# Kernel tuning notes

Hardware: AMD Instinct MI355X
Metric: run time of the kernel (lower is better)

The kernel has to match this reference:

```python
import jax, jax.numpy as jnp
import numpy as np

N = 20000   # nodes per graph
E = 320000  # edges per graph
D_IN, D_H = 128, 304


def _param(key, shape, fan_in):
    return jax.random.normal(key, shape, dtype=jnp.float32) / np.sqrt(fan_in)


def setup_inputs() -> dict:
    key = jax.random.key(0)
    ks = jax.random.split(key, 20)
    inp = {}
    for i, name in enumerate(['x1', 'x2', 'x3']):
        inp[name] = jax.random.normal(ks[i], (N, D_IN), dtype=jnp.float32)
    for i, name in enumerate(['src1', 'dst1', 'src2', 'dst2', 'src3', 'dst3']):
        inp[name] = jax.random.randint(ks[3 + i], (E,), 0, N, dtype=jnp.int32)
    # shared GraphConv weights (DGL GraphConv: h = norm_agg(x) @ W + b)
    inp['W1'] = _param(ks[9], (D_IN, D_H), D_IN)
    inp['b1'] = jnp.zeros((D_H,), jnp.float32)
    inp['W2'] = _param(ks[10], (D_H, D_H), D_H)
    inp['b2'] = jnp.zeros((D_H,), jnp.float32)
    inp['W3'] = _param(ks[11], (D_H, D_H), D_H)
    inp['b3'] = jnp.zeros((D_H,), jnp.float32)
    # MLP head: 304 -> 128 -> 64 -> 1
    inp['fW1'] = _param(ks[12], (D_H, 128), D_H)
    inp['fb1'] = jnp.zeros((128,), jnp.float32)
    inp['fW2'] = _param(ks[13], (128, 64), 128)
    inp['fb2'] = jnp.zeros((64,), jnp.float32)
    inp['fW3'] = _param(ks[14], (64, 1), 64)
    inp['fb3'] = jnp.zeros((1,), jnp.float32)
    return inp


def gcn_conv(x, src, dst, W, b):
    # DGL GraphConv, norm='both': h = D_in^{-1/2} A D_out^{-1/2} x W + b
    ones = jnp.ones((src.shape[0],), x.dtype)
    out_deg = jnp.clip(jax.ops.segment_sum(ones, src, num_segments=N), 1.0)
    in_deg = jnp.clip(jax.ops.segment_sum(ones, dst, num_segments=N), 1.0)
    h = x * jax.lax.rsqrt(out_deg)[:, None]
    agg = jax.ops.segment_sum(h[src], dst, num_segments=N)  # [N, d] SpMM
    agg = agg * jax.lax.rsqrt(in_deg)[:, None]
    return agg @ W + b


def reference(x1, x2, x3, src1, dst1, src2, dst2, src3, dst3,
              W1, b1, W2, b2, W3, b3, fW1, fb1, fW2, fb2, fW3, fb3):
    def branch(x, src, dst):
        x = jax.nn.relu(gcn_conv(x, src, dst, W1, b1))
        x = jax.nn.relu(gcn_conv(x, src, dst, W2, b2))
        x = jax.nn.relu(gcn_conv(x, src, dst, W3, b3))
        return x

    h1 = branch(x1, src1, dst1)
    h2 = branch(x2, src2, dst2)
    h3 = branch(x3, src3, dst3)
    # multi_graph_opt='max': max over all nodes of all three graphs -> [304]
    pooled = jnp.max(jnp.concatenate([h1, h2, h3], axis=0), axis=0)
    # output_opt='fc': MLP head with sigmoid
    z = jax.nn.relu(pooled @ fW1 + fb1)
    z = jax.nn.relu(z @ fW2 + fb2)
    return jax.nn.sigmoid(z @ fW3 + fb3)  # shape [1]
```

## Files before the change

### kernel.cpp

```cpp
#include <hip/hip_runtime.h>
#include <hip/hip_bf16.h>
#include <math.h>

#define NODES 20000
#define EDGES 320000
#define NB 3
#define TOTN (NODES * NB)
#define TOTE (EDGES * NB)
#define D_IN 128
#define D_H 304
#define SCAN_B 59
#define SLICES 40
#define SLICE_E (EDGES / SLICES)
#define ZX TOTN
#define ZQ (TOTN + 96)
#define OFFB 237
#define PACKB 7500
#define PREPWB 912

typedef __attribute__((ext_vector_type(4))) float f32x4;
typedef __attribute__((ext_vector_type(2))) float f32x2;

__device__ __forceinline__ void gload16(const void* g, void* l) {
    __builtin_amdgcn_global_load_lds(
        (const __attribute__((address_space(1))) unsigned*)g,
        (__attribute__((address_space(3))) unsigned*)l, 16, 0, 0);
}

__global__ __launch_bounds__(256, 1) void k_hist(
    const int* __restrict__ s1, const int* __restrict__ d1,
    const int* __restrict__ s2, const int* __restrict__ d2,
    const int* __restrict__ s3, const int* __restrict__ d3,
    unsigned short* __restrict__ partial_in, unsigned short* __restrict__ partial_out,
    int* __restrict__ gctr) {
    __shared__ unsigned hist[NODES / 2];
    if (blockIdx.x == 0 && blockIdx.y == 0 && threadIdx.x == 0) *gctr = 0;
    int g = blockIdx.x / SLICES, s = blockIdx.x % SLICES;
    bool isOut = (blockIdx.y == 1);
    const int* ep;
    if (isOut) ep = (g == 0) ? s1 : ((g == 1) ? s2 : s3);
    else       ep = (g == 0) ? d1 : ((g == 1) ? d2 : d3);
    ep += s * SLICE_E;
    for (int i = threadIdx.x; i < NODES / 2; i += 256) hist[i] = 0;
    __syncthreads();
    const int4* ep4 = (const int4*)ep;
    for (int i = threadIdx.x; i < SLICE_E / 4; i += 256) {
        int4 v = ep4[i];
        atomicAdd(&hist[v.x >> 1], 1u << ((v.x & 1) << 4));
        atomicAdd(&hist[v.y >> 1], 1u << ((v.y & 1) << 4));
        atomicAdd(&hist[v.z >> 1], 1u << ((v.z & 1) << 4));
        atomicAdd(&hist[v.w >> 1], 1u << ((v.w & 1) << 4));
    }
    __syncthreads();
    unsigned* po = (unsigned*)((isOut ? partial_out : partial_in) + (size_t)blockIdx.x * NODES);
    for (int i = threadIdx.x; i < NODES / 2; i += 256) po[i] = hist[i];
}

__global__ void k_degscan(const unsigned short* __restrict__ partial_in,
                          const unsigned short* __restrict__ partial_out,
                          float* __restrict__ inv_in, float* __restrict__ inv_out,
                          int* __restrict__ row_ptr, int* __restrict__ rend,
                          int* __restrict__ gctr) {
    __shared__ int wsum[16];
    __shared__ int sbase;
    int b = blockIdx.x, t = threadIdx.x;
    int i = b * 1024 + t;
    int lane = t & 63, wid = t >> 6;
    int v = 0;
    if (i < TOTN) {
        int g = i / NODES, ln = i - g * NODES;
        const unsigned short* pi = partial_in + (size_t)g * SLICES * NODES + ln;
        const unsigned short* po = partial_out + (size_t)g * SLICES * NODES + ln;
        int ci = 0, co = 0;
        #pragma unroll
        for (int s = 0; s < SLICES; s++) { ci += pi[s * NODES]; co += po[s * NODES]; }
        v = ci;
        inv_in[i]  = 1.0f / sqrtf((float)max(ci, 1));
        inv_out[i] = 1.0f / sqrtf((float)max(co, 1));
    }
    int sv = v;
    #pragma unroll
    for (int o = 1; o < 64; o <<= 1) {
        int u = __shfl_up(sv, o, 64);
        if (lane >= o) sv += u;
    }
    if (lane == 63) wsum[wid] = sv;
    __syncthreads();
    if (t < 16) {
        int w = wsum[t];
        #pragma unroll
        for (int o = 1; o < 16; o <<= 1) {
            int u = __shfl_up(w, o, 16);
            if (t >= o) w += u;
        }
        wsum[t] = w;
    }
    __syncthreads();
    if (t == 0) sbase = atomicAdd(gctr, wsum[15]);
    __syncthreads();
    int wbase = (wid > 0) ? wsum[wid - 1] : 0;
    if (i < TOTN) {
        int rp = sbase + wbase + sv - v;
        row_ptr[i] = rp;
        rend[i] = rp + v;
    }
}

__global__ void k_prep(const int* __restrict__ row_ptr,
                       const unsigned short* __restrict__ partial_in,
                       int* __restrict__ O,
                       int* __restrict__ csr_slack, unsigned* __restrict__ x8z,
                       unsigned* __restrict__ q8z, int* __restrict__ pooled,
                       const float4* __restrict__ x1, const float4* __restrict__ x2,
                       const float4* __restrict__ x3, const float* __restrict__ inv_out,
                       unsigned* __restrict__ q,
                       const float* __restrict__ W1, const float* __restrict__ W2,
                       const float* __restrict__ W3,
                       unsigned char* __restrict__ Wt1, unsigned char* __restrict__ Wt2,
                       unsigned char* __restrict__ Wt3) {
    if (blockIdx.x < OFFB) {
        int n = blockIdx.x * 256 + threadIdx.x;
        if (n >= TOTN) {
            int ex = n - TOTN;
            if (ex < 32) csr_slack[ex] = 0;
            else if (ex < 64) x8z[ex - 32] = 0;
            else if (ex < 144) q8z[ex - 64] = 0;
            else if (ex < 464) pooled[ex - 144] = 0;
            return;
        }
        int rp = row_ptr[n];
        int g = n / NODES, ln = n - g * NODES;
        const unsigned short* pi = partial_in + (size_t)g * SLICES * NODES + ln;
        int* on = O + (size_t)g * SLICES * NODES + ln;
        int run = rp;
        #pragma unroll
        for (int s = 0; s < SLICES; s++) {
            on[s * NODES] = run;
            run += pi[s * NODES];
        }
    } else if (blockIdx.x < OFFB + PACKB) {
        const int per = NODES * D_IN / 4;
        int i = (blockIdx.x - OFFB) * 256 + threadIdx.x;
        const float4* s; int j;
        if (i < per)          { s = x1; j = i; }
        else if (i < 2 * per) { s = x2; j = i - per; }
        else                  { s = x3; j = i - 2 * per; }
        float4 v = s[j];
        float sc = inv_out[i >> 5];
        int p = __builtin_amdgcn_cvt_pk_fp8_f32(v.x * sc, v.y * sc, 0, false);
        p = __builtin_amdgcn_cvt_pk_fp8_f32(v.z * sc, v.w * sc, p, true);
        q[i] = (unsigned)p;
    } else {
        const int N1 = D_H * 128, N2 = D_H * 320;
        int id = (blockIdx.x - OFFB - PACKB) * 256 + threadIdx.x;
        const float* W; unsigned char* Wt; int K, Kpad, lid;
        if (id < N1)                { W = W1; Wt = Wt1; K = 128; Kpad = 128; lid = id; }
        else if (id < N1 + N2)      { W = W2; Wt = Wt2; K = 304; Kpad = 320; lid = id - N1; }
        else                        { W = W3; Wt = Wt3; K = 304; Kpad = 320; lid = id - N1 - N2; }
        int n = lid / Kpad, k = lid - n * Kpad;
        unsigned char v = 0;
        if (k < K) {
            float w = W[k * D_H + n];
            v = (unsigned char)(__builtin_amdgcn_cvt_pk_fp8_f32(w, w, 0, false) & 0xff);
        }
        Wt[lid] = v;
    }
}

__global__ __launch_bounds__(256, 1) void k_fill2(
    const int* __restrict__ s1, const int* __restrict__ d1,
    const int* __restrict__ s2, const int* __restrict__ d2,
    const int* __restrict__ s3, const int* __restrict__ d3,
    const int* __restrict__ O, int* __restrict__ csr) {
    __shared__ int cur[NODES];
    int g = blockIdx.x / SLICES, s = blockIdx.x % SLICES;
    const int* sp = (g == 0) ? s1 : ((g == 1) ? s2 : s3);
    const int* dp = (g == 0) ? d1 : ((g == 1) ? d2 : d3);
    sp += s * SLICE_E; dp += s * SLICE_E;
    const int* on = O + (size_t)blockIdx.x * NODES;
    for (int i = threadIdx.x; i < NODES; i += 256) cur[i] = on[i];
    __syncthreads();
    int base = g * NODES;
    const int4* sp4 = (const int4*)sp;
    const int4* dp4 = (const int4*)dp;
    for (int i = threadIdx.x; i < SLICE_E / 4; i += 256) {
        int4 dv = dp4[i];
        int4 sv = sp4[i];
        int p0 = atomicAdd(&cur[dv.x], 1); csr[p0] = sv.x + base;
        int p1 = atomicAdd(&cur[dv.y], 1); csr[p1] = sv.y + base;
        int p2 = atomicAdd(&cur[dv.z], 1); csr[p2] = sv.z + base;
        int p3 = atomicAdd(&cur[dv.w], 1); csr[p3] = sv.w + base;
    }
}

__global__ void k_spmm_l1(const uint2* __restrict__ h, unsigned char* __restrict__ agg,
                          const int* __restrict__ row_ptr, const int* __restrict__ rend,
                          const int* __restrict__ csr,
                          const float* __restrict__ inv_in) {
    int n = blockIdx.x * 4 + (threadIdx.x >> 6);
    int lane = threadIdx.x & 63;
    int s = lane >> 4;
    int off = lane & 15;
    f32x2 a[4];
    #pragma unroll
    for (int j = 0; j < 4; j++) a[j] = (f32x2){0.f, 0.f};
    int k0 = row_ptr[n], k1 = rend[n];
    int deg = k1 - k0;
    const int* cp = csr + k0 + s;
    int e[8];
    #pragma unroll
    for (int j = 0; j < 8; j++) {
        int ev = cp[4 * j];
        e[j] = (s + 4 * j < deg) ? ev : ZX;
    }
    uint2 u[8];
    #pragma unroll
    for (int j = 0; j < 8; j++)
        if (4 * j < deg) u[j] = h[(size_t)e[j] * 16 + off];
    #pragma unroll
    for (int j = 0; j < 8; j++) {
        if (4 * j < deg) {
            a[0] += __builtin_amdgcn_cvt_pk_f32_fp8(u[j].x, false);
            a[1] += __builtin_amdgcn_cvt_pk_f32_fp8(u[j].x, true);
            a[2] += __builtin_amdgcn_cvt_pk_f32_fp8(u[j].y, false);
            a[3] += __builtin_amdgcn_cvt_pk_f32_fp8(u[j].y, true);
        }
    }
    for (int k = k0 + 32 + s; k < k1; k += 4) {
        int e0 = csr[k];
        uint2 u0 = h[(size_t)e0 * 16 + off];
        a[0] += __builtin_amdgcn_cvt_pk_f32_fp8(u0.x, false);
        a[1] += __builtin_amdgcn_cvt_pk_f32_fp8(u0.x, true);
        a[2] += __builtin_amdgcn_cvt_pk_f32_fp8(u0.y, false);
        a[3] += __builtin_amdgcn_cvt_pk_f32_fp8(u0.y, true);
    }
    float r[8];
    #pragma unroll
    for (int j = 0; j < 4; j++) {
        #pragma unroll
        for (int c = 0; c < 2; c++) {
            float v = a[j][c];
            r[2 * j + c] = v + __shfl(v, lane + 16, 64)
                             + __shfl(v, lane + 32, 64)
                             + __shfl(v, lane + 48, 64);
        }
    }
    if (lane < 16) {
        float wi = inv_in[n];
        int d0 = __builtin_amdgcn_cvt_pk_fp8_f32(r[0] * wi, r[1] * wi, 0, false);
        d0 = __builtin_amdgcn_cvt_pk_fp8_f32(r[2] * wi, r[3] * wi, d0, true);
        int d1 = __builtin_amdgcn_cvt_pk_fp8_f32(r[4] * wi, r[5] * wi, 0, false);
        d1 = __builtin_amdgcn_cvt_pk_fp8_f32(r[6] * wi, r[7] * wi, d1, true);
        uint2 st; st.x = (unsigned)d0; st.y = (unsigned)d1;
        *(uint2*)(agg + (size_t)n * 128 + lane * 8) = st;
    }
}

__global__ void k_spmm_big(const uint4* __restrict__ h, unsigned char* __restrict__ agg,
                           const int* __restrict__ row_ptr, const int* __restrict__ rend,
                           const int* __restrict__ csr,
                           const float* __restrict__ inv_in) {
    int n = blockIdx.x * 4 + (threadIdx.x >> 6);
    int lane = threadIdx.x & 63;
    int s = lane / 20;
    int off = lane % 20;
    f32x2 a[8];
    #pragma unroll
    for (int j = 0; j < 8; j++) a[j] = (f32x2){0.f, 0.f};
    int k0 = row_ptr[n], k1 = rend[n];
    int deg = k1 - k0;
    int degg = (s < 3) ? deg : 0;
    const int* cp = csr + k0 + s;
    int e[8];
    #pragma unroll
    for (int j = 0; j < 8; j++) {
        int ev = cp[3 * j];
        e[j] = (s + 3 * j < degg) ? ev : ZQ;
    }
    uint4 u[8];
    #pragma unroll
    for (int j = 0; j < 8; j++)
        if (3 * j < deg) u[j] = h[(size_t)e[j] * 20 + off];
    #pragma unroll
    for (int j = 0; j < 8; j++) {
        if (3 * j < deg) {
            a[0] += __builtin_amdgcn_cvt_pk_f32_fp8(u[j].x, false);
            a[1] += __builtin_amdgcn_cvt_pk_f32_fp8(u[j].x, true);
            a[2] += __builtin_amdgcn_cvt_pk_f32_fp8(u[j].y, false);
            a[3] += __builtin_amdgcn_cvt_pk_f32_fp8(u[j].y, true);
            a[4] += __builtin_amdgcn_cvt_pk_f32_fp8(u[j].z, false);
            a[5] += __builtin_amdgcn_cvt_pk_f32_fp8(u[j].z, true);
            a[6] += __builtin_amdgcn_cvt_pk_f32_fp8(u[j].w, false);
            a[7] += __builtin_amdgcn_cvt_pk_f32_fp8(u[j].w, true);
        }
    }
    int k1g = k0 + degg;
    for (int k = k0 + 24 + s; k < k1g; k += 3) {
        int e0 = csr[k];
        uint4 u0 = h[(size_t)e0 * 20 + off];
        a[0] += __builtin_amdgcn_cvt_pk_f32_fp8(u0.x, false);
        a[1] += __builtin_amdgcn_cvt_pk_f32_fp8(u0.x, true);
        a[2] += __builtin_amdgcn_cvt_pk_f32_fp8(u0.y, false);
        a[3] += __builtin_amdgcn_cvt_pk_f32_fp8(u0.y, true);
        a[4] += __builtin_amdgcn_cvt_pk_f32_fp8(u0.z, false);
        a[5] += __builtin_amdgcn_cvt_pk_f32_fp8(u0.z, true);
        a[6] += __builtin_amdgcn_cvt_pk_f32_fp8(u0.w, false);
        a[7] += __builtin_amdgcn_cvt_pk_f32_fp8(u0.w, true);
    }
    float r[16];
    #pragma unroll
    for (int j = 0; j < 8; j++) {
        #pragma unroll
        for (int c = 0; c < 2; c++) {
            float v = a[j][c];
            r[2 * j + c] = v + __shfl(v, lane + 20, 64) + __shfl(v, lane + 40, 64);
        }
    }
    if (lane < 20) {
        float wi = inv_in[n];
        int d0 = __builtin_amdgcn_cvt_pk_fp8_f32(r[0] * wi, r[1] * wi, 0, false);
        d0 = __builtin_amdgcn_cvt_pk_fp8_f32(r[2] * wi, r[3] * wi, d0, true);
        int d1 = __builtin_amdgcn_cvt_pk_fp8_f32(r[4] * wi, r[5] * wi, 0, false);
        d1 = __builtin_amdgcn_cvt_pk_fp8_f32(r[6] * wi, r[7] * wi, d1, true);
        int d2 = __builtin_amdgcn_cvt_pk_fp8_f32(r[8] * wi, r[9] * wi, 0, false);
        d2 = __builtin_amdgcn_cvt_pk_fp8_f32(r[10] * wi, r[11] * wi, d2, true);
        int d3 = __builtin_amdgcn_cvt_pk_fp8_f32(r[12] * wi, r[13] * wi, 0, false);
        d3 = __builtin_amdgcn_cvt_pk_fp8_f32(r[14] * wi, r[15] * wi, d3, true);
        uint4 st; st.x = (unsigned)d0; st.y = (unsigned)d1; st.z = (unsigned)d2; st.w = (unsigned)d3;
        *(uint4*)(agg + (size_t)n * 320 + lane * 16) = st;
    }
}

template <int MODE>
__global__ __launch_bounds__(256, 2) void k_gemm_mfma(
    const unsigned char* __restrict__ A, int lda,
    const unsigned char* __restrict__ Wt,
    const float* __restrict__ bias,
    const float* __restrict__ inv_out,
    unsigned char* __restrict__ C8, int* __restrict__ gpool, int M, int K) {
    __shared__ char SM[55296];
    __shared__ int pmax[D_H];
    int tid = threadIdx.x;
    int wv = tid >> 6, lane = tid & 63;
    int quad = lane >> 4, lrow = lane & 15;
    int bm = blockIdx.x * 128;

    if (MODE == 1) {
        for (int i = tid; i < D_H; i += 256) pmax[i] = 0;
    }

    f32x4 acc[2][19];
    #pragma unroll
    for (int r = 0; r < 2; r++)
        #pragma unroll
        for (int t = 0; t < 19; t++) acc[r][t] = (f32x4){0.f, 0.f, 0.f, 0.f};

    int swz = (lrow & 3) ^ (lrow >> 2);
    int hb = (quad & 1) * 8;

    auto stage = [&](int buf, int kt) {
        char* As = SM + buf * 27648;
        char* Bs = As + 8192;
        #pragma unroll
        for (int j = 0; j < 2; j++) {
            int c = j * 256 + tid;
            int row = c >> 2, xc = c & 3;
            int col = xc ^ (row & 3) ^ ((row >> 2) & 3);
            gload16(A + (size_t)(bm + row) * lda + kt + col * 16, As + c * 16);
        }
        #pragma unroll
        for (int j = 0; j < 5; j++) {
            int c = j * 256 + tid;
            if (c < 1216) {
                int row = c >> 2, xc = c & 3;
                int col = xc ^ (row & 3) ^ ((row >> 2) & 3);
                gload16(Wt + (size_t)row * K + kt + col * 16, Bs + c * 16);
            }
        }
    };

    int nt = K >> 6;
    stage(0, 0);
    __syncthreads();
    for (int t = 0; t < nt; t++) {
        if (t + 1 < nt) stage((t + 1) & 1, (t + 1) << 6);
        const char* As = SM + (t & 1) * 27648;
        const char* Bs = As + 8192;
        #pragma unroll
        for (int sub = 0; sub < 2; sub++) {
            int c0 = sub * 2 + (quad >> 1);
            int cx = (c0 ^ swz) * 16 + hb;
            int ra = wv * 32 + lrow;
            long long a0 = *(const long long*)(As + ra * 64 + cx);
            long long a1 = *(const long long*)(As + (ra + 16) * 64 + cx);
            #pragma unroll
            for (int u = 0; u < 19; u++) {
                long long b = *(const long long*)(Bs + (u * 16 + lrow) * 64 + cx);
                acc[0][u] = __builtin_amdgcn_mfma_f32_16x16x32_fp8_fp8(a0, b, acc[0][u], 0, 0, 0);
                acc[1][u] = __builtin_amdgcn_mfma_f32_16x16x32_fp8_fp8(a1, b, acc[1][u], 0, 0, 0);
            }
        }
        __syncthreads();
    }
    if (MODE == 0) {
        unsigned char* OUT = (unsigned char*)SM;
        if (tid < 128) *(uint4*)(OUT + tid * 320 + 304) = make_uint4(0u, 0u, 0u, 0u);
        #pragma unroll
        for (int t = 0; t < 19; t++) {
            int col = t * 16 + lrow;
            float bv = bias[col];
            #pragma unroll
            for (int r = 0; r < 2; r++) {
                int rl = wv * 32 + r * 16 + quad * 4;
                #pragma unroll
                for (int g = 0; g < 4; g++) {
                    int row = bm + rl + g;
                    float sc = inv_out[min(row, M - 1)];
                    float v = fmaxf(acc[r][t][g] + bv, 0.f) * sc;
                    int p = __builtin_amdgcn_cvt_pk_fp8_f32(v, v, 0, false);
                    OUT[(rl + g) * 320 + col] = (unsigned char)(p & 0xff);
                }
            }
        }
        __syncthreads();
        #pragma unroll
        for (int j = 0; j < 10; j++) {
            int c = j * 256 + tid;
            *(uint4*)(C8 + (size_t)bm * 320 + (size_t)c * 16) = *(const uint4*)(OUT + c * 16);
        }
    } else {
        #pragma unroll
        for (int t = 0; t < 19; t++) {
            int col = t * 16 + lrow;
            float bv = bias[col];
            float m = 0.f;
            #pragma unroll
            for (int r = 0; r < 2; r++) {
                int rbase = bm + wv * 32 + r * 16 + quad * 4;
                #pragma unroll
                for (int g = 0; g < 4; g++) {
                    int row = rbase + g;
                    if (row < M) m = fmaxf(m, fmaxf(acc[r][t][g] + bv, 0.f));
                }
            }
            atomicMax(&pmax[col], __float_as_int(m));
        }
        __syncthreads();
        for (int i = tid; i < D_H; i += 256)
            atomicMax(&gpool[i], pmax[i]);
    }
}

__global__ void k_mlp(const int* __restrict__ pooled_i,
                      const float* __restrict__ fW1, const float* __restrict__ fb1,
                      const float* __restrict__ fW2, const float* __restrict__ fb2,
                      const float* __restrict__ fW3, const float* __restrict__ fb3,
                      float* __restrict__ out) {
    __shared__ float p[D_H];
    __shared__ float z1[128];
    __shared__ float z2[64];
    int t = threadIdx.x;
    if (t < D_H) p[t] = __int_as_float(pooled_i[t]);
    __syncthreads();
    if (t < 128) {
        float acc = fb1[t];
        for (int k = 0; k < D_H; k++) acc += p[k] * fW1[k * 128 + t];
        z1[t] = fmaxf(acc, 0.f);
    }
    __syncthreads();
    if (t < 64) {
        float acc = fb2[t];
        for (int k = 0; k < 128; k++) acc += z1[k] * fW2[k * 64 + t];
        z2[t] = fmaxf(acc, 0.f);
    }
    __syncthreads();
    if (t == 0) {
        float acc = fb3[0];
        for (int k = 0; k < 64; k++) acc += z2[k] * fW3[k];
        out[0] = 1.f / (1.f + expf(-acc));
    }
}

extern "C" void kernel_launch(void* const* d_in, const int* in_sizes, int n_in,
                              void* d_out, int out_size, void* d_ws, size_t ws_size,
                              hipStream_t stream) {
    const float* x1 = (const float*)d_in[0];
    const float* x2 = (const float*)d_in[1];
    const float* x3 = (const float*)d_in[2];
    const int* src1 = (const int*)d_in[3];
    const int* dst1 = (const int*)d_in[4];
    const int* src2 = (const int*)d_in[5];
    const int* dst2 = (const int*)d_in[6];
    const int* src3 = (const int*)d_in[7];
    const int* dst3 = (const int*)d_in[8];
    const float* W1 = (const float*)d_in[9];
    const float* b1 = (const float*)d_in[10];
    const float* W2 = (const float*)d_in[11];
    const float* b2 = (const float*)d_in[12];
    const float* W3 = (const float*)d_in[13];
    const float* b3 = (const float*)d_in[14];
    const float* fW1 = (const float*)d_in[15];
    const float* fb1 = (const float*)d_in[16];
    const float* fW2 = (const float*)d_in[17];
    const float* fb2 = (const float*)d_in[18];
    const float* fW3 = (const float*)d_in[19];
    const float* fb3 = (const float*)d_in[20];
    float* out = (float*)d_out;

    char* w = (char*)d_ws;
    unsigned* X8       = (unsigned*)w;      w += (size_t)(TOTN + 1) * 32 * 4;
    unsigned char* Q8  = (unsigned char*)w; w += (size_t)(TOTN + 128) * 320;
    unsigned char* P8  = (unsigned char*)w; w += (size_t)(TOTN + 128) * 320;
    unsigned char* Wt1 = (unsigned char*)w; w += (size_t)D_H * 128;
    unsigned char* Wt2 = (unsigned char*)w; w += (size_t)D_H * 320;
    unsigned char* Wt3 = (unsigned char*)w; w += (size_t)D_H * 320;
    w = (char*)(((size_t)w + 255) & ~(size_t)255);
    unsigned short* partial_in  = (unsigned short*)w; w += (size_t)NB * SLICES * NODES * 2;
    unsigned short* partial_out = (unsigned short*)w; w += (size_t)NB * SLICES * NODES * 2;
    int* O         = (int*)w;    w += (size_t)NB * SLICES * NODES * 4;
    float* inv_out = (float*)w;  w += (size_t)TOTN * 4;
    float* inv_in  = (float*)w;  w += (size_t)TOTN * 4;
    int* row_ptr   = (int*)w;    w += (size_t)TOTN * 4;
    int* rend      = (int*)w;    w += (size_t)TOTN * 4;
    int* csr       = (int*)w;    w += (size_t)(TOTE + 32) * 4;
    int* pooled    = (int*)w;    w += 320 * 4;
    int* gctr      = (int*)w;    w += 64;

    k_hist<<<dim3(NB * SLICES, 2), 256, 0, stream>>>(src1, dst1, src2, dst2, src3, dst3,
                                                     partial_in, partial_out, gctr);
    k_degscan<<<SCAN_B, 1024, 0, stream>>>(partial_in, partial_out,
                                           inv_in, inv_out, row_ptr, rend, gctr);
    k_prep<<<OFFB + PACKB + PREPWB, 256, 0, stream>>>(
        row_ptr, partial_in, O, csr + TOTE,
        X8 + (size_t)ZX * 32, (unsigned*)(Q8 + (size_t)ZQ * 320), pooled,
        (const float4*)x1, (const float4*)x2, (const float4*)x3, inv_out, X8,
        W1, W2, W3, Wt1, Wt2, Wt3);
    k_fill2<<<NB * SLICES, 256, 0, stream>>>(src1, dst1, src2, dst2, src3, dst3, O, csr);

    int ggrid = (TOTN + 127) / 128;

    k_spmm_l1<<<TOTN / 4, 256, 0, stream>>>((const uint2*)X8, P8, row_ptr, rend, csr, inv_in);
    k_gemm_mfma<0><<<ggrid, 256, 0, stream>>>(P8, 128, Wt1, b1, inv_out,
                                              Q8, nullptr, TOTN, 128);
    k_spmm_big<<<TOTN / 4, 256, 0, stream>>>((const uint4*)Q8, P8, row_ptr, rend, csr, inv_in);
    k_gemm_mfma<0><<<ggrid, 256, 0, stream>>>(P8, 320, Wt2, b2, inv_out,
                                              Q8, nullptr, TOTN, 320);
    k_spmm_big<<<TOTN / 4, 256, 0, stream>>>((const uint4*)Q8, P8, row_ptr, rend, csr, inv_in);
    k_gemm_mfma<1><<<ggrid, 256, 0, stream>>>(P8, 320, Wt3, b3, nullptr,
                                              nullptr, pooled, TOTN, 320);

    k_mlp<<<1, 320, 0, stream>>>(pooled, fW1, fb1, fW2, fb2, fW3, fb3, out);
}
```

Measured before the change: 322.5 us.

## Map one node per 16/20-lane group in SpMM and widen histogram blocks

The SpMM kernels switch from one wavefront per node, with edges split across lane groups and a shuffle reduction, to one node per lane group. Each group walks that node's edges serially with two-stage double-buffered gathers. This removes the cross-lane shuffle reduction and the idle lanes on low-degree nodes, at the cost of longer serial edge loops and divergence when degrees vary within a wave. Separately, the histogram and CSR-fill kernels move to 1024-thread blocks, and the weight-transpose buffers are padded to 320 rows so the GEMM B staging loses its bounds check.

```diff
diff --git a/kernel.cpp b/kernel.cpp
--- a/kernel.cpp
+++ b/kernel.cpp
@@ -16,7 +16,7 @@
 #define ZQ (TOTN + 96)
 #define OFFB 237
 #define PACKB 7500
-#define PREPWB 912
+#define PREPWB 960
 
 typedef __attribute__((ext_vector_type(4))) float f32x4;
 typedef __attribute__((ext_vector_type(2))) float f32x2;
@@ -27,7 +27,7 @@
         (__attribute__((address_space(3))) unsigned*)l, 16, 0, 0);
 }
 
-__global__ __launch_bounds__(256, 1) void k_hist(
+__global__ __launch_bounds__(1024, 1) void k_hist(
     const int* __restrict__ s1, const int* __restrict__ d1,
     const int* __restrict__ s2, const int* __restrict__ d2,
     const int* __restrict__ s3, const int* __restrict__ d3,
@@ -41,10 +41,10 @@
     if (isOut) ep = (g == 0) ? s1 : ((g == 1) ? s2 : s3);
     else       ep = (g == 0) ? d1 : ((g == 1) ? d2 : d3);
     ep += s * SLICE_E;
-    for (int i = threadIdx.x; i < NODES / 2; i += 256) hist[i] = 0;
+    for (int i = threadIdx.x; i < NODES / 2; i += 1024) hist[i] = 0;
     __syncthreads();
     const int4* ep4 = (const int4*)ep;
-    for (int i = threadIdx.x; i < SLICE_E / 4; i += 256) {
+    for (int i = threadIdx.x; i < SLICE_E / 4; i += 1024) {
         int4 v = ep4[i];
         atomicAdd(&hist[v.x >> 1], 1u << ((v.x & 1) << 4));
         atomicAdd(&hist[v.y >> 1], 1u << ((v.y & 1) << 4));
@@ -53,7 +53,7 @@
     }
     __syncthreads();
     unsigned* po = (unsigned*)((isOut ? partial_out : partial_in) + (size_t)blockIdx.x * NODES);
-    for (int i = threadIdx.x; i < NODES / 2; i += 256) po[i] = hist[i];
+    for (int i = threadIdx.x; i < NODES / 2; i += 1024) po[i] = hist[i];
 }
 
 __global__ void k_degscan(const unsigned short* __restrict__ partial_in,
@@ -151,7 +151,7 @@
         p = __builtin_amdgcn_cvt_pk_fp8_f32(v.z * sc, v.w * sc, p, true);
         q[i] = (unsigned)p;
     } else {
-        const int N1 = D_H * 128, N2 = D_H * 320;
+        const int N1 = 320 * 128, N2 = 320 * 320;
         int id = (blockIdx.x - OFFB - PACKB) * 256 + threadIdx.x;
         const float* W; unsigned char* Wt; int K, Kpad, lid;
         if (id < N1)                { W = W1; Wt = Wt1; K = 128; Kpad = 128; lid = id; }
@@ -159,7 +159,7 @@
         else                        { W = W3; Wt = Wt3; K = 304; Kpad = 320; lid = id - N1 - N2; }
         int n = lid / Kpad, k = lid - n * Kpad;
         unsigned char v = 0;
-        if (k < K) {
+        if (k < K && n < D_H) {
             float w = W[k * D_H + n];
             v = (unsigned char)(__builtin_amdgcn_cvt_pk_fp8_f32(w, w, 0, false) & 0xff);
         }
@@ -167,7 +167,7 @@
     }
 }
 
-__global__ __launch_bounds__(256, 1) void k_fill2(
+__global__ __launch_bounds__(1024, 1) void k_fill2(
     const int* __restrict__ s1, const int* __restrict__ d1,
     const int* __restrict__ s2, const int* __restrict__ d2,
     const int* __restrict__ s3, const int* __restrict__ d3,
@@ -178,12 +178,12 @@
     const int* dp = (g == 0) ? d1 : ((g == 1) ? d2 : d3);
     sp += s * SLICE_E; dp += s * SLICE_E;
     const int* on = O + (size_t)blockIdx.x * NODES;
-    for (int i = threadIdx.x; i < NODES; i += 256) cur[i] = on[i];
+    for (int i = threadIdx.x; i < NODES; i += 1024) cur[i] = on[i];
     __syncthreads();
     int base = g * NODES;
     const int4* sp4 = (const int4*)sp;
     const int4* dp4 = (const int4*)dp;
-    for (int i = threadIdx.x; i < SLICE_E / 4; i += 256) {
+    for (int i = threadIdx.x; i < SLICE_E / 4; i += 1024) {
         int4 dv = dp4[i];
         int4 sv = sp4[i];
         int p0 = atomicAdd(&cur[dv.x], 1); csr[p0] = sv.x + base;
@@ -197,106 +197,111 @@
                           const int* __restrict__ row_ptr, const int* __restrict__ rend,
                           const int* __restrict__ csr,
                           const float* __restrict__ inv_in) {
-    int n = blockIdx.x * 4 + (threadIdx.x >> 6);
-    int lane = threadIdx.x & 63;
-    int s = lane >> 4;
+    int tid = threadIdx.x;
+    int wv = tid >> 6, lane = tid & 63;
+    int grp = lane >> 4;
     int off = lane & 15;
+    int n = blockIdx.x * 16 + wv * 4 + grp;
+    int k0 = row_ptr[n];
+    int deg = rend[n] - k0;
+    const int* cp = csr + k0;
     f32x2 a[4];
     #pragma unroll
     for (int j = 0; j < 4; j++) a[j] = (f32x2){0.f, 0.f};
-    int k0 = row_ptr[n], k1 = rend[n];
-    int deg = k1 - k0;
-    const int* cp = csr + k0 + s;
+    uint2 ua[8], ub[8];
     int e[8];
-    #pragma unroll
-    for (int j = 0; j < 8; j++) {
-        int ev = cp[4 * j];
-        e[j] = (s + 4 * j < deg) ? ev : ZX;
-    }
-    uint2 u[8];
-    #pragma unroll
-    for (int j = 0; j < 8; j++)
-        if (4 * j < deg) u[j] = h[(size_t)e[j] * 16 + off];
-    #pragma unroll
-    for (int j = 0; j < 8; j++) {
-        if (4 * j < deg) {
-            a[0] += __builtin_amdgcn_cvt_pk_f32_fp8(u[j].x, false);
-            a[1] += __builtin_amdgcn_cvt_pk_f32_fp8(u[j].x, true);
-            a[2] += __builtin_amdgcn_cvt_pk_f32_fp8(u[j].y, false);
-            a[3] += __builtin_amdgcn_cvt_pk_f32_fp8(u[j].y, true);
-        }
-    }
-    for (int k = k0 + 32 + s; k < k1; k += 4) {
-        int e0 = csr[k];
+    #define L1_LOAD(dst, base)                                        \
+        { _Pragma("unroll")                                           \
+          for (int j = 0; j < 8; j++) {                               \
+              int ev = cp[(base) + j];                                \
+              e[j] = ((base) + j < deg) ? ev : ZX;                    \
+          }                                                           \
+          _Pragma("unroll")                                           \
+          for (int j = 0; j < 8; j++)                                 \
+              dst[j] = h[(size_t)e[j] * 16 + off]; }
+    #define L1_ACC(src)                                               \
+        { _Pragma("unroll")                                           \
+          for (int j = 0; j < 8; j++) {                               \
+              a[0] += __builtin_amdgcn_cvt_pk_f32_fp8(src[j].x, false); \
+              a[1] += __builtin_amdgcn_cvt_pk_f32_fp8(src[j].x, true);  \
+              a[2] += __builtin_amdgcn_cvt_pk_f32_fp8(src[j].y, false); \
+              a[3] += __builtin_amdgcn_cvt_pk_f32_fp8(src[j].y, true); } }
+    bool n3 = __any(deg > 16);
+    bool n4 = __any(deg > 24);
+    L1_LOAD(ua, 0)
+    L1_LOAD(ub, 8)
+    L1_ACC(ua)
+    if (n3) L1_LOAD(ua, 16)
+    L1_ACC(ub)
+    if (n4) L1_LOAD(ub, 24)
+    if (n3) L1_ACC(ua)
+    if (n4) L1_ACC(ub)
+    for (int k = 32; k < deg; k++) {
+        int e0 = cp[k];
         uint2 u0 = h[(size_t)e0 * 16 + off];
         a[0] += __builtin_amdgcn_cvt_pk_f32_fp8(u0.x, false);
         a[1] += __builtin_amdgcn_cvt_pk_f32_fp8(u0.x, true);
         a[2] += __builtin_amdgcn_cvt_pk_f32_fp8(u0.y, false);
         a[3] += __builtin_amdgcn_cvt_pk_f32_fp8(u0.y, true);
     }
-    float r[8];
-    #pragma unroll
-    for (int j = 0; j < 4; j++) {
-        #pragma unroll
-        for (int c = 0; c < 2; c++) {
-            float v = a[j][c];
-            r[2 * j + c] = v + __shfl(v, lane + 16, 64)
-                             + __shfl(v, lane + 32, 64)
-                             + __shfl(v, lane + 48, 64);
-        }
-    }
-    if (lane < 16) {
-        float wi = inv_in[n];
-        int d0 = __builtin_amdgcn_cvt_pk_fp8_f32(r[0] * wi, r[1] * wi, 0, false);
-        d0 = __builtin_amdgcn_cvt_pk_fp8_f32(r[2] * wi, r[3] * wi, d0, true);
-        int d1 = __builtin_amdgcn_cvt_pk_fp8_f32(r[4] * wi, r[5] * wi, 0, false);
-        d1 = __builtin_amdgcn_cvt_pk_fp8_f32(r[6] * wi, r[7] * wi, d1, true);
-        uint2 st; st.x = (unsigned)d0; st.y = (unsigned)d1;
-        *(uint2*)(agg + (size_t)n * 128 + lane * 8) = st;
-    }
+    #undef L1_LOAD
+    #undef L1_ACC
+    float wi = inv_in[n];
+    int d0 = __builtin_amdgcn_cvt_pk_fp8_f32(a[0][0] * wi, a[0][1] * wi, 0, false);
+    d0 = __builtin_amdgcn_cvt_pk_fp8_f32(a[1][0] * wi, a[1][1] * wi, d0, true);
+    int d1 = __builtin_amdgcn_cvt_pk_fp8_f32(a[2][0] * wi, a[2][1] * wi, 0, false);
+    d1 = __builtin_amdgcn_cvt_pk_fp8_f32(a[3][0] * wi, a[3][1] * wi, d1, true);
+    uint2 st; st.x = (unsigned)d0; st.y = (unsigned)d1;
+    *(uint2*)(agg + (size_t)n * 128 + off * 8) = st;
 }
 
 __global__ void k_spmm_big(const uint4* __restrict__ h, unsigned char* __restrict__ agg,
                            const int* __restrict__ row_ptr, const int* __restrict__ rend,
                            const int* __restrict__ csr,
                            const float* __restrict__ inv_in) {
-    int n = blockIdx.x * 4 + (threadIdx.x >> 6);
-    int lane = threadIdx.x & 63;
-    int s = lane / 20;
+    int tid = threadIdx.x;
+    int wv = tid >> 6, lane = tid & 63;
+    int grp = lane / 20;
     int off = lane % 20;
+    bool act = grp < 3;
+    int n = blockIdx.x * 12 + wv * 3 + (act ? grp : 0);
+    int k0 = row_ptr[n];
+    int deg = act ? (rend[n] - k0) : 0;
+    const int* cp = csr + k0;
     f32x2 a[8];
     #pragma unroll
     for (int j = 0; j < 8; j++) a[j] = (f32x2){0.f, 0.f};
-    int k0 = row_ptr[n], k1 = rend[n];
-    int deg = k1 - k0;
-    int degg = (s < 3) ? deg : 0;
-    const int* cp = csr + k0 + s;
+    uint4 ua[8], ub[8];
     int e[8];
-    #pragma unroll
-    for (int j = 0; j < 8; j++) {
-        int ev = cp[3 * j];
-        e[j] = (s + 3 * j < degg) ? ev : ZQ;
-    }
-    uint4 u[8];
-    #pragma unroll
-    for (int j = 0; j < 8; j++)
-        if (3 * j < deg) u[j] = h[(size_t)e[j] * 20 + off];
-    #pragma unroll
-    for (int j = 0; j < 8; j++) {
-        if (3 * j < deg) {
-            a[0] += __builtin_amdgcn_cvt_pk_f32_fp8(u[j].x, false);
-            a[1] += __builtin_amdgcn_cvt_pk_f32_fp8(u[j].x, true);
-            a[2] += __builtin_amdgcn_cvt_pk_f32_fp8(u[j].y, false);
-            a[3] += __builtin_amdgcn_cvt_pk_f32_fp8(u[j].y, true);
-            a[4] += __builtin_amdgcn_cvt_pk_f32_fp8(u[j].z, false);
-            a[5] += __builtin_amdgcn_cvt_pk_f32_fp8(u[j].z, true);
-            a[6] += __builtin_amdgcn_cvt_pk_f32_fp8(u[j].w, false);
-            a[7] += __builtin_amdgcn_cvt_pk_f32_fp8(u[j].w, true);
-        }
-    }
-    int k1g = k0 + degg;
-    for (int k = k0 + 24 + s; k < k1g; k += 3) {
-        int e0 = csr[k];
+    #define BG_LOAD(dst, base)                                        \
+        { _Pragma("unroll")                                           \
+          for (int j = 0; j < 8; j++) {                               \
+              int ev = cp[(base) + j];                                \
+              e[j] = ((base) + j < deg) ? ev : ZQ;                    \
+          }                                                           \
+          _Pragma("unroll")                                           \
+          for (int j = 0; j < 8; j++)                                 \
+              dst[j] = h[(size_t)e[j] * 20 + off]; }
+    #define BG_ACC(src)                                               \
+        { _Pragma("unroll")                                           \
+          for (int j = 0; j < 8; j++) {                               \
+              a[0] += __builtin_amdgcn_cvt_pk_f32_fp8(src[j].x, false); \
+              a[1] += __builtin_amdgcn_cvt_pk_f32_fp8(src[j].x, true);  \
+              a[2] += __builtin_amdgcn_cvt_pk_f32_fp8(src[j].y, false); \
+              a[3] += __builtin_amdgcn_cvt_pk_f32_fp8(src[j].y, true);  \
+              a[4] += __builtin_amdgcn_cvt_pk_f32_fp8(src[j].z, false); \
+              a[5] += __builtin_amdgcn_cvt_pk_f32_fp8(src[j].z, true);  \
+              a[6] += __builtin_amdgcn_cvt_pk_f32_fp8(src[j].w, false); \
+              a[7] += __builtin_amdgcn_cvt_pk_f32_fp8(src[j].w, true); } }
+    bool n3 = __any(deg > 16);
+    BG_LOAD(ua, 0)
+    BG_LOAD(ub, 8)
+    BG_ACC(ua)
+    if (n3) BG_LOAD(ua, 16)
+    BG_ACC(ub)
+    if (n3) BG_ACC(ua)
+    for (int k = 24; k < deg; k++) {
+        int e0 = cp[k];
         uint4 u0 = h[(size_t)e0 * 20 + off];
         a[0] += __builtin_amdgcn_cvt_pk_f32_fp8(u0.x, false);
         a[1] += __builtin_amdgcn_cvt_pk_f32_fp8(u0.x, true);
@@ -307,27 +312,20 @@
         a[6] += __builtin_amdgcn_cvt_pk_f32_fp8(u0.w, false);
         a[7] += __builtin_amdgcn_cvt_pk_f32_fp8(u0.w, true);
     }
-    float r[16];
-    #pragma unroll
-    for (int j = 0; j < 8; j++) {
-        #pragma unroll
-        for (int c = 0; c < 2; c++) {
-            float v = a[j][c];
-            r[2 * j + c] = v + __shfl(v, lane + 20, 64) + __shfl(v, lane + 40, 64);
-        }
-    }
-    if (lane < 20) {
+    #undef BG_LOAD
+    #undef BG_ACC
+    if (act) {
         float wi = inv_in[n];
-        int d0 = __builtin_amdgcn_cvt_pk_fp8_f32(r[0] * wi, r[1] * wi, 0, false);
-        d0 = __builtin_amdgcn_cvt_pk_fp8_f32(r[2] * wi, r[3] * wi, d0, true);
-        int d1 = __builtin_amdgcn_cvt_pk_fp8_f32(r[4] * wi, r[5] * wi, 0, false);
-        d1 = __builtin_amdgcn_cvt_pk_fp8_f32(r[6] * wi, r[7] * wi, d1, true);
-        int d2 = __builtin_amdgcn_cvt_pk_fp8_f32(r[8] * wi, r[9] * wi, 0, false);
-        d2 = __builtin_amdgcn_cvt_pk_fp8_f32(r[10] * wi, r[11] * wi, d2, true);
-        int d3 = __builtin_amdgcn_cvt_pk_fp8_f32(r[12] * wi, r[13] * wi, 0, false);
-        d3 = __builtin_amdgcn_cvt_pk_fp8_f32(r[14] * wi, r[15] * wi, d3, true);
+        int d0 = __builtin_amdgcn_cvt_pk_fp8_f32(a[0][0] * wi, a[0][1] * wi, 0, false);
+        d0 = __builtin_amdgcn_cvt_pk_fp8_f32(a[1][0] * wi, a[1][1] * wi, d0, true);
+        int d1 = __builtin_amdgcn_cvt_pk_fp8_f32(a[2][0] * wi, a[2][1] * wi, 0, false);
+        d1 = __builtin_amdgcn_cvt_pk_fp8_f32(a[3][0] * wi, a[3][1] * wi, d1, true);
+        int d2 = __builtin_amdgcn_cvt_pk_fp8_f32(a[4][0] * wi, a[4][1] * wi, 0, false);
+        d2 = __builtin_amdgcn_cvt_pk_fp8_f32(a[5][0] * wi, a[5][1] * wi, d2, true);
+        int d3 = __builtin_amdgcn_cvt_pk_fp8_f32(a[6][0] * wi, a[6][1] * wi, 0, false);
+        d3 = __builtin_amdgcn_cvt_pk_fp8_f32(a[7][0] * wi, a[7][1] * wi, d3, true);
         uint4 st; st.x = (unsigned)d0; st.y = (unsigned)d1; st.z = (unsigned)d2; st.w = (unsigned)d3;
-        *(uint4*)(agg + (size_t)n * 320 + lane * 16) = st;
+        *(uint4*)(agg + (size_t)n * 320 + off * 16) = st;
     }
 }
 
@@ -338,7 +336,7 @@
     const float* __restrict__ bias,
     const float* __restrict__ inv_out,
     unsigned char* __restrict__ C8, int* __restrict__ gpool, int M, int K) {
-    __shared__ char SM[55296];
+    __shared__ char SM[57344];
     __shared__ int pmax[D_H];
     int tid = threadIdx.x;
     int wv = tid >> 6, lane = tid & 63;
@@ -359,7 +357,7 @@
     int hb = (quad & 1) * 8;
 
     auto stage = [&](int buf, int kt) {
-        char* As = SM + buf * 27648;
+        char* As = SM + buf * 28672;
         char* Bs = As + 8192;
         #pragma unroll
         for (int j = 0; j < 2; j++) {
@@ -371,11 +369,9 @@
         #pragma unroll
         for (int j = 0; j < 5; j++) {
             int c = j * 256 + tid;
-            if (c < 1216) {
-                int row = c >> 2, xc = c & 3;
-                int col = xc ^ (row & 3) ^ ((row >> 2) & 3);
-                gload16(Wt + (size_t)row * K + kt + col * 16, Bs + c * 16);
-            }
+            int row = c >> 2, xc = c & 3;
+            int col = xc ^ (row & 3) ^ ((row >> 2) & 3);
+            gload16(Wt + (size_t)row * K + kt + col * 16, Bs + c * 16);
         }
     };
 
@@ -384,7 +380,7 @@
     __syncthreads();
     for (int t = 0; t < nt; t++) {
         if (t + 1 < nt) stage((t + 1) & 1, (t + 1) << 6);
-        const char* As = SM + (t & 1) * 27648;
+        const char* As = SM + (t & 1) * 28672;
         const char* Bs = As + 8192;
         #pragma unroll
         for (int sub = 0; sub < 2; sub++) {
@@ -511,9 +507,9 @@
     unsigned* X8       = (unsigned*)w;      w += (size_t)(TOTN + 1) * 32 * 4;
     unsigned char* Q8  = (unsigned char*)w; w += (size_t)(TOTN + 128) * 320;
     unsigned char* P8  = (unsigned char*)w; w += (size_t)(TOTN + 128) * 320;
-    unsigned char* Wt1 = (unsigned char*)w; w += (size_t)D_H * 128;
-    unsigned char* Wt2 = (unsigned char*)w; w += (size_t)D_H * 320;
-    unsigned char* Wt3 = (unsigned char*)w; w += (size_t)D_H * 320;
+    unsigned char* Wt1 = (unsigned char*)w; w += (size_t)320 * 128;
+    unsigned char* Wt2 = (unsigned char*)w; w += (size_t)320 * 320;
+    unsigned char* Wt3 = (unsigned char*)w; w += (size_t)320 * 320;
     w = (char*)(((size_t)w + 255) & ~(size_t)255);
     unsigned short* partial_in  = (unsigned short*)w; w += (size_t)NB * SLICES * NODES * 2;
     unsigned short* partial_out = (unsigned short*)w; w += (size_t)NB * SLICES * NODES * 2;
@@ -526,8 +522,8 @@
     int* pooled    = (int*)w;    w += 320 * 4;
     int* gctr      = (int*)w;    w += 64;
 
-    k_hist<<<dim3(NB * SLICES, 2), 256, 0, stream>>>(src1, dst1, src2, dst2, src3, dst3,
-                                                     partial_in, partial_out, gctr);
+    k_hist<<<dim3(NB * SLICES, 2), 1024, 0, stream>>>(src1, dst1, src2, dst2, src3, dst3,
+                                                      partial_in, partial_out, gctr);
     k_degscan<<<SCAN_B, 1024, 0, stream>>>(partial_in, partial_out,
                                            inv_in, inv_out, row_ptr, rend, gctr);
     k_prep<<<OFFB + PACKB + PREPWB, 256, 0, stream>>>(
@@ -535,17 +531,17 @@
         X8 + (size_t)ZX * 32, (unsigned*)(Q8 + (size_t)ZQ * 320), pooled,
         (const float4*)x1, (const float4*)x2, (const float4*)x3, inv_out, X8,
         W1, W2, W3, Wt1, Wt2, Wt3);
-    k_fill2<<<NB * SLICES, 256, 0, stream>>>(src1, dst1, src2, dst2, src3, dst3, O, csr);
+    k_fill2<<<NB * SLICES, 1024, 0, stream>>>(src1, dst1, src2, dst2, src3, dst3, O, csr);
 
     int ggrid = (TOTN + 127) / 128;
 
-    k_spmm_l1<<<TOTN / 4, 256, 0, stream>>>((const uint2*)X8, P8, row_ptr, rend, csr, inv_in);
+    k_spmm_l1<<<TOTN / 16, 256, 0, stream>>>((const uint2*)X8, P8, row_ptr, rend, csr, inv_in);
     k_gemm_mfma<0><<<ggrid, 256, 0, stream>>>(P8, 128, Wt1, b1, inv_out,
                                               Q8, nullptr, TOTN, 128);
-    k_spmm_big<<<TOTN / 4, 256, 0, stream>>>((const uint4*)Q8, P8, row_ptr, rend, csr, inv_in);
+    k_spmm_big<<<TOTN / 12, 256, 0, stream>>>((const uint4*)Q8, P8, row_ptr, rend, csr, inv_in);
     k_gemm_mfma<0><<<ggrid, 256, 0, stream>>>(P8, 320, Wt2, b2, inv_out,
                                               Q8, nullptr, TOTN, 320);
-    k_spmm_big<<<TOTN / 4, 256, 0, stream>>>((const uint4*)Q8, P8, row_ptr, rend, csr, inv_in);
+    k_spmm_big<<<TOTN / 12, 256, 0, stream>>>((const uint4*)Q8, P8, row_ptr, rend, csr, inv_in);
     k_gemm_mfma<1><<<ggrid, 256, 0, stream>>>(P8, 320, Wt3, b3, nullptr,
                                               nullptr, pooled, TOTN, 320);
 
```

After: 393.6 us. 1.22x slower.
